# Kernel optimization log

Hardware: AMD Instinct MI355X
Metric: run time of the kernel (lower is better)

The kernel has to match this reference:

```python
import jax, jax.numpy as jnp
import numpy as np

MAX_SEQ_LEN = 2048
H, K = 16, 8
D_IN, D_OUT = 1024, 1024
D_H, D_O = D_IN // H, D_OUT // H


def _get_phi(L, K):
    # Hankel matrix Z[i,j] = 2 / ((i+j)^3 - (i+j) + 1e-7), 1-indexed
    e = np.arange(1, L + 1, dtype=np.float64)
    s = e[:, None] + e[None, :]
    Z = 2.0 / (s ** 3 - s + 1e-7)
    sigma, phi = np.linalg.eigh(Z)
    sigma, phi = sigma[-K:], phi[:, -K:]
    phi = phi * sigma ** 0.25
    return jnp.asarray(phi, dtype=jnp.float32)  # (L, K)


def setup_inputs() -> dict:
    key = jax.random.key(0)
    k_x, k_w, k_d = jax.random.split(key, 3)
    B, T = 4, 2048
    x = jax.random.normal(k_x, (B, T, D_IN), dtype=jnp.float32)
    # kaiming_uniform(a=sqrt(5)) on (H,K,d_h,d_o): fan_in = K*d_h*d_o, bound = 1/sqrt(fan_in)
    fan_in = K * D_H * D_O
    bound = 1.0 / np.sqrt(fan_in)
    weight = jax.random.uniform(k_w, (H, K, D_H, D_O), minval=-bound, maxval=bound, dtype=jnp.float32)
    # torch init is zeros; use small random so the score path is exercised
    diag = 0.02 * jax.random.normal(k_d, (K, D_IN), dtype=jnp.float32)
    phi = _get_phi(MAX_SEQ_LEN, K)
    return {"x": x, "weight": weight, "diag": diag, "phi": phi}


def reference(x, weight, diag, phi):
    B, T, _ = x.shape
    Hh, Kk, d_h, d_o = weight.shape
    # scores: (B, T, K) = phi[:T] broadcast + x @ diag^T
    scores = phi[:T][None, :, :] + jnp.einsum('bti,ki->btk', x, diag)
    xh = x.reshape(B, T, Hh, d_h).transpose(0, 2, 1, 3)  # (B, H, T, d_h)
    # per-head, per-expert GEMM -> (B, H, K, T, d_o)
    y = jnp.einsum('bhti,hkio->bhkto', xh, weight)
    # score-weighted combine over experts -> (B, T, H, d_o)
    y = jnp.einsum('bhkto,btk->btho', y, scores)
    return y.reshape(B, T, Hh * d_o)
```

## Files before the change

kernel.cpp:

```cpp
#include <hip/hip_runtime.h>
#include <hip/hip_bf16.h>

#define BT    8192
#define SEQ_T 2048
#define DIN   1024
#define NH    16
#define NK    8
#define DH    64
#define DO    64

typedef __bf16 bf16;
typedef __attribute__((ext_vector_type(8))) __bf16 bf16x8;
typedef __attribute__((ext_vector_type(4))) __bf16 bf16x4;
typedef __attribute__((ext_vector_type(4))) float floatx4;

__global__ __launch_bounds__(256) void prep_kernel(
    const float* __restrict__ x, const float* __restrict__ weight,
    const float* __restrict__ diag, const float* __restrict__ phi,
    float* __restrict__ scores_t, bf16* __restrict__ wt, bf16* __restrict__ xh)
{
  int blk = blockIdx.x, tid = threadIdx.x;
  if (blk < BT / 4) {
    int wave = tid >> 6, lane = tid & 63;
    int token = blk * 4 + wave;
    const floatx4* xr = (const floatx4*)(x + (size_t)token * DIN);
    const floatx4* dg = (const floatx4*)diag;
    floatx4 acc[NK];
#pragma unroll
    for (int k = 0; k < NK; k++) acc[k] = (floatx4){0.f, 0.f, 0.f, 0.f};
#pragma unroll
    for (int it = 0; it < 4; it++) {
      floatx4 xv = xr[it * 64 + lane];
      int col = it * 256 + lane * 4;
      int h = col >> 6, c = col & 63;
      bf16x4 cv;
      cv[0] = (bf16)xv[0]; cv[1] = (bf16)xv[1];
      cv[2] = (bf16)xv[2]; cv[3] = (bf16)xv[3];
      *(bf16x4*)(xh + ((size_t)h * BT + token) * 64 + c) = cv;
#pragma unroll
      for (int k = 0; k < NK; k++) {
        floatx4 dv = dg[k * 256 + it * 64 + lane];
        acc[k] += xv * dv;
      }
    }
    float r[NK];
#pragma unroll
    for (int k = 0; k < NK; k++)
      r[k] = (acc[k][0] + acc[k][1]) + (acc[k][2] + acc[k][3]);
#pragma unroll
    for (int k = 0; k < NK; k++) {
      float v = r[k];
#pragma unroll
      for (int off = 32; off >= 1; off >>= 1) v += __shfl_xor(v, off, 64);
      r[k] = v;
    }
    if (lane == 0) {
      int t = token & (SEQ_T - 1);
#pragma unroll
      for (int k = 0; k < NK; k++)
        scores_t[(size_t)k * BT + token] = phi[t * NK + k] + r[k];
    }
  } else {
    __shared__ bf16 tile[64 * 68];
    int hk = blk - BT / 4;
    const float* wsrc = weight + (size_t)hk * DH * DO;
#pragma unroll
    for (int it = 0; it < 4; it++) {
      int idx = it * 1024 + tid * 4;
      int i = idx >> 6, o = idx & 63;
      floatx4 v = *(const floatx4*)(wsrc + idx);
#pragma unroll
      for (int r = 0; r < 4; r++)
        tile[(o + r) * 68 + i] = (bf16)v[r];
    }
    __syncthreads();
#pragma unroll
    for (int it = 0; it < 4; it++) {
      int idx = it * 1024 + tid * 4;
      int o2 = idx >> 6, i2 = idx & 63;
      bf16x4 v = *(const bf16x4*)&tile[o2 * 68 + i2];
      *(bf16x4*)(wt + (size_t)hk * 4096 + idx) = v;
    }
  }
}

__global__ __launch_bounds__(256, 3) void moe_kernel(
    const bf16* __restrict__ xh, const bf16* __restrict__ wt,
    const float* __restrict__ scores_t, float* __restrict__ out)
{
  __shared__ bf16  xl[128 * 64];
  __shared__ bf16  wl[256 * 64];
  __shared__ float sl[NK * 128];

  int bid = blockIdx.x;
  int g  = bid >> 5;
  int h  = (bid >> 1) & 15;
  int nh = bid & 1;
  int tid = threadIdx.x, lane = tid & 63, w = tid >> 6;
  int l15 = lane & 15, q = lane >> 4;

  {
    const bf16* xs = xh + ((size_t)h * BT + g * 128) * 64;
#pragma unroll
    for (int it = 0; it < 4; it++) {
      int idx = it * 256 + tid;
      int row = idx >> 3, c = idx & 7, pc = c ^ (row & 7);
      bf16x8 v = *(const bf16x8*)(xs + idx * 8);
      *(bf16x8*)(xl + row * 64 + pc * 8) = v;
    }
  }
  {
#pragma unroll
    for (int it = 0; it < 8; it++) {
      int idx = it * 256 + tid;
      int R = idx >> 3, c = idx & 7;
      int e = R >> 5, o = R & 31;
      bf16x8 v = *(const bf16x8*)(wt + ((size_t)(h * NK + e) * DO + nh * 32 + o) * 64 + c * 8);
      int pc = c ^ (R & 7);
      *(bf16x8*)(wl + R * 64 + pc * 8) = v;
    }
  }
  {
    int k = tid >> 5, t4 = (tid & 31) * 4;
    floatx4 v = *(const floatx4*)(scores_t + (size_t)k * BT + g * 128 + t4);
    *(floatx4*)(sl + k * 128 + t4) = v;
  }
  __syncthreads();

  int mh = w >> 1;
  int ns = w & 1;

  bf16x8 b[NK][2];
#pragma unroll
  for (int e = 0; e < NK; e++) {
    int R = e * 32 + ns * 16 + l15;
#pragma unroll
    for (int ki = 0; ki < 2; ki++) {
      int pc = (ki * 4 + q) ^ (R & 7);
      b[e][ki] = *(const bf16x8*)(wl + R * 64 + pc * 8);
    }
  }

#pragma unroll
  for (int m = 0; m < 4; m++) {
    int tr = mh * 64 + m * 16;
    int row = tr + l15;
    int p0 = q ^ (row & 7), p1 = (q + 4) ^ (row & 7);
    bf16x8 a0 = *(const bf16x8*)(xl + row * 64 + p0 * 8);
    bf16x8 a1 = *(const bf16x8*)(xl + row * 64 + p1 * 8);
    floatx4 y = (floatx4){0.f, 0.f, 0.f, 0.f};
#pragma unroll
    for (int e = 0; e < NK; e++) {
      floatx4 s4 = *(const floatx4*)(sl + e * 128 + tr + q * 4);
      floatx4 z = (floatx4){0.f, 0.f, 0.f, 0.f};
      z = __builtin_amdgcn_mfma_f32_16x16x32_bf16(a0, b[e][0], z, 0, 0, 0);
      z = __builtin_amdgcn_mfma_f32_16x16x32_bf16(a1, b[e][1], z, 0, 0, 0);
      y += s4 * z;
    }
    int orow = g * 128 + tr + q * 4;
    float* op = out + (size_t)orow * (NH * DO) + h * DO + nh * 32 + ns * 16 + l15;
#pragma unroll
    for (int r = 0; r < 4; r++)
      op[(size_t)r * (NH * DO)] = y[r];
  }
}

extern "C" void kernel_launch(void* const* d_in, const int* in_sizes, int n_in,
                              void* d_out, int out_size, void* d_ws, size_t ws_size,
                              hipStream_t stream) {
  const float* x      = (const float*)d_in[0];
  const float* weight = (const float*)d_in[1];
  const float* diag   = (const float*)d_in[2];
  const float* phi    = (const float*)d_in[3];
  float* out = (float*)d_out;

  bf16*  wt       = (bf16*)d_ws;
  float* scores_t = (float*)((char*)d_ws + (2u << 20));
  bf16*  xh       = (bf16*)((char*)d_ws + (4u << 20));

  prep_kernel<<<BT / 4 + NH * NK, 256, 0, stream>>>(x, weight, diag, phi,
                                                    scores_t, wt, xh);
  moe_kernel<<<64 * NH * 2, 256, 0, stream>>>(xh, wt, scores_t, out);
}
```

Baseline: 108.6 us.

## Make MoE blocks persistent over four token tiles with double-buffered prefetch

Each moe_kernel block now handles four 128-token chunks instead of one, so the expert weight tile is loaded into shared memory once and reused across them. The next chunk's x and scores are prefetched into registers and written to a second LDS buffer while the current chunk computes. Block IDs are also remapped so that neighbouring blocks land on different XCDs, and launch bounds drop to 2 blocks per CU. Grid size falls from 2048 to 512 blocks, which reduces weight reloads and exposed load latency but risks lower occupancy and less parallelism.

```diff
diff --git a/kernel.cpp b/kernel.cpp
--- a/kernel.cpp
+++ b/kernel.cpp
@@ -84,52 +84,55 @@
   }
 }
 
-__global__ __launch_bounds__(256, 3) void moe_kernel(
+__global__ __launch_bounds__(256, 2) void moe_kernel(
     const bf16* __restrict__ xh, const bf16* __restrict__ wt,
     const float* __restrict__ scores_t, float* __restrict__ out)
 {
-  __shared__ bf16  xl[128 * 64];
   __shared__ bf16  wl[256 * 64];
-  __shared__ float sl[NK * 128];
-
-  int bid = blockIdx.x;
-  int g  = bid >> 5;
-  int h  = (bid >> 1) & 15;
-  int nh = bid & 1;
+  __shared__ bf16  xl[2][128 * 64];
+  __shared__ float sl[2][NK * 128];
+
+  int lid = ((blockIdx.x & 7) << 6) | (blockIdx.x >> 3);
+  int nh    = lid & 1;
+  int chunk = (lid >> 1) & 15;
+  int h     = lid >> 5;
   int tid = threadIdx.x, lane = tid & 63, w = tid >> 6;
   int l15 = lane & 15, q = lane >> 4;
 
-  {
-    const bf16* xs = xh + ((size_t)h * BT + g * 128) * 64;
-#pragma unroll
-    for (int it = 0; it < 4; it++) {
-      int idx = it * 256 + tid;
-      int row = idx >> 3, c = idx & 7, pc = c ^ (row & 7);
-      bf16x8 v = *(const bf16x8*)(xs + idx * 8);
-      *(bf16x8*)(xl + row * 64 + pc * 8) = v;
-    }
-  }
-  {
-#pragma unroll
-    for (int it = 0; it < 8; it++) {
-      int idx = it * 256 + tid;
-      int R = idx >> 3, c = idx & 7;
-      int e = R >> 5, o = R & 31;
-      bf16x8 v = *(const bf16x8*)(wt + ((size_t)(h * NK + e) * DO + nh * 32 + o) * 64 + c * 8);
-      int pc = c ^ (R & 7);
-      *(bf16x8*)(wl + R * 64 + pc * 8) = v;
-    }
-  }
-  {
-    int k = tid >> 5, t4 = (tid & 31) * 4;
-    floatx4 v = *(const floatx4*)(scores_t + (size_t)k * BT + g * 128 + t4);
-    *(floatx4*)(sl + k * 128 + t4) = v;
-  }
+  const bf16*  xs = xh + ((size_t)h * BT + chunk * 512) * 64;
+  const float* ss = scores_t + chunk * 512;
+  int sk = tid >> 5, st4 = (tid & 31) * 4;
+
+  bf16x8 wv[8];
+#pragma unroll
+  for (int it = 0; it < 8; it++) {
+    int idx = it * 256 + tid, R = idx >> 3, c = idx & 7;
+    int e = R >> 5, o = R & 31;
+    wv[it] = *(const bf16x8*)(wt +
+        (((size_t)(h * NK + e)) * DO + nh * 32 + o) * 64 + c * 8);
+  }
+  bf16x8 xv[4];
+#pragma unroll
+  for (int it = 0; it < 4; it++)
+    xv[it] = *(const bf16x8*)(xs + (it * 256 + tid) * 8);
+  floatx4 sv = *(const floatx4*)(ss + (size_t)sk * BT + st4);
+
+#pragma unroll
+  for (int it = 0; it < 8; it++) {
+    int idx = it * 256 + tid, R = idx >> 3, c = idx & 7;
+    int pc = c ^ (R & 7);
+    *(bf16x8*)(wl + R * 64 + pc * 8) = wv[it];
+  }
+#pragma unroll
+  for (int it = 0; it < 4; it++) {
+    int idx = it * 256 + tid, row = idx >> 3, c = idx & 7, pc = c ^ (row & 7);
+    *(bf16x8*)(xl[0] + row * 64 + pc * 8) = xv[it];
+  }
+  *(floatx4*)(sl[0] + sk * 128 + st4) = sv;
   __syncthreads();
 
   int mh = w >> 1;
   int ns = w & 1;
-
   bf16x8 b[NK][2];
 #pragma unroll
   for (int e = 0; e < NK; e++) {
@@ -142,26 +145,59 @@
   }
 
 #pragma unroll
-  for (int m = 0; m < 4; m++) {
-    int tr = mh * 64 + m * 16;
-    int row = tr + l15;
-    int p0 = q ^ (row & 7), p1 = (q + 4) ^ (row & 7);
-    bf16x8 a0 = *(const bf16x8*)(xl + row * 64 + p0 * 8);
-    bf16x8 a1 = *(const bf16x8*)(xl + row * 64 + p1 * 8);
-    floatx4 y = (floatx4){0.f, 0.f, 0.f, 0.f};
-#pragma unroll
-    for (int e = 0; e < NK; e++) {
-      floatx4 s4 = *(const floatx4*)(sl + e * 128 + tr + q * 4);
-      floatx4 z = (floatx4){0.f, 0.f, 0.f, 0.f};
-      z = __builtin_amdgcn_mfma_f32_16x16x32_bf16(a0, b[e][0], z, 0, 0, 0);
-      z = __builtin_amdgcn_mfma_f32_16x16x32_bf16(a1, b[e][1], z, 0, 0, 0);
-      y += s4 * z;
-    }
-    int orow = g * 128 + tr + q * 4;
-    float* op = out + (size_t)orow * (NH * DO) + h * DO + nh * 32 + ns * 16 + l15;
-#pragma unroll
-    for (int r = 0; r < 4; r++)
-      op[(size_t)r * (NH * DO)] = y[r];
+  for (int i = 0; i < 4; i++) {
+    const bf16*  xlc = xl[i & 1];
+    const float* slc = sl[i & 1];
+
+    if (i < 3) {
+#pragma unroll
+      for (int it = 0; it < 4; it++)
+        xv[it] = *(const bf16x8*)(xs + (i + 1) * (128 * 64) +
+                                  (it * 256 + tid) * 8);
+      sv = *(const floatx4*)(ss + (size_t)sk * BT + (i + 1) * 128 + st4);
+    }
+
+    floatx4 yy[4];
+#pragma unroll
+    for (int m = 0; m < 4; m++) {
+      int tr = mh * 64 + m * 16;
+      int row = tr + l15;
+      int p0 = q ^ (row & 7), p1 = (q + 4) ^ (row & 7);
+      bf16x8 a0 = *(const bf16x8*)(xlc + row * 64 + p0 * 8);
+      bf16x8 a1 = *(const bf16x8*)(xlc + row * 64 + p1 * 8);
+      floatx4 y = (floatx4){0.f, 0.f, 0.f, 0.f};
+#pragma unroll
+      for (int e = 0; e < NK; e++) {
+        floatx4 s4 = *(const floatx4*)(slc + e * 128 + tr + q * 4);
+        floatx4 z = (floatx4){0.f, 0.f, 0.f, 0.f};
+        z = __builtin_amdgcn_mfma_f32_16x16x32_bf16(a0, b[e][0], z, 0, 0, 0);
+        z = __builtin_amdgcn_mfma_f32_16x16x32_bf16(a1, b[e][1], z, 0, 0, 0);
+        y += s4 * z;
+      }
+      yy[m] = y;
+    }
+
+    if (i < 3) {
+#pragma unroll
+      for (int it = 0; it < 4; it++) {
+        int idx = it * 256 + tid, row = idx >> 3, c = idx & 7;
+        int pc = c ^ (row & 7);
+        *(bf16x8*)(xl[(i + 1) & 1] + row * 64 + pc * 8) = xv[it];
+      }
+      *(floatx4*)(sl[(i + 1) & 1] + sk * 128 + st4) = sv;
+      __syncthreads();
+    }
+
+#pragma unroll
+    for (int m = 0; m < 4; m++) {
+      int tr = mh * 64 + m * 16;
+      int orow = (chunk * 4 + i) * 128 + tr + q * 4;
+      float* op = out + (size_t)orow * (NH * DO) + h * DO +
+                  nh * 32 + ns * 16 + l15;
+#pragma unroll
+      for (int r = 0; r < 4; r++)
+        op[(size_t)r * (NH * DO)] = yy[m][r];
+    }
   }
 }
 
@@ -180,5 +216,5 @@
 
   prep_kernel<<<BT / 4 + NH * NK, 256, 0, stream>>>(x, weight, diag, phi,
                                                     scores_t, wt, xh);
-  moe_kernel<<<64 * NH * 2, 256, 0, stream>>>(xh, wt, scores_t, out);
+  moe_kernel<<<512, 256, 0, stream>>>(xh, wt, scores_t, out);
 }
```

Measured after the change: 110.0 us. No clear change (+1.3%).

## Pre-swizzle LDS images in prep and load via direct global-to-LDS DMA

Applied to the files above, without the earlier changes.

The prep kernel now writes x and weight already in the XOR-swizzled per-block LDS layout, so the MoE kernel can copy them with contiguous global_load_lds 16-byte transfers that skip the register round-trip. Scores are loaded the same way. The block index is also permuted so that consecutive blocks land on different XCDs, which changes L2 locality. This removes VGPR staging and address arithmetic from the load phase, but it relies on how global_load_lds places data for each lane. It also assumes the 16-byte LDS load is supported on this target.

```diff
diff --git a/kernel.cpp b/kernel.cpp
--- a/kernel.cpp
+++ b/kernel.cpp
@@ -14,15 +14,22 @@
 typedef __attribute__((ext_vector_type(4))) __bf16 bf16x4;
 typedef __attribute__((ext_vector_type(4))) float floatx4;
 
+#define GLOAD_LDS16(gp, lp)                                        \
+  __builtin_amdgcn_global_load_lds(                                \
+      (__attribute__((address_space(1))) const void*)(gp),         \
+      (__attribute__((address_space(3))) void*)(lp), 16, 0, 0)
+
 __global__ __launch_bounds__(256) void prep_kernel(
     const float* __restrict__ x, const float* __restrict__ weight,
     const float* __restrict__ diag, const float* __restrict__ phi,
-    float* __restrict__ scores_t, bf16* __restrict__ wt, bf16* __restrict__ xh)
+    float* __restrict__ scores_t, bf16* __restrict__ wimg,
+    bf16* __restrict__ ximg)
 {
   int blk = blockIdx.x, tid = threadIdx.x;
   if (blk < BT / 4) {
     int wave = tid >> 6, lane = tid & 63;
     int token = blk * 4 + wave;
+    int row = token & 127, gg = token >> 7;
     const floatx4* xr = (const floatx4*)(x + (size_t)token * DIN);
     const floatx4* dg = (const floatx4*)diag;
     floatx4 acc[NK];
@@ -36,7 +43,8 @@
       bf16x4 cv;
       cv[0] = (bf16)xv[0]; cv[1] = (bf16)xv[1];
       cv[2] = (bf16)xv[2]; cv[3] = (bf16)xv[3];
-      *(bf16x4*)(xh + ((size_t)h * BT + token) * 64 + c) = cv;
+      int a = (((c >> 3) ^ (row & 7)) << 3) + (c & 7);
+      *(bf16x4*)(ximg + ((size_t)(gg * 16 + h) * 128 + row) * 64 + a) = cv;
 #pragma unroll
       for (int k = 0; k < NK; k++) {
         floatx4 dv = dg[k * 256 + it * 64 + lane];
@@ -63,6 +71,7 @@
   } else {
     __shared__ bf16 tile[64 * 68];
     int hk = blk - BT / 4;
+    int h = hk >> 3, k = hk & 7;
     const float* wsrc = weight + (size_t)hk * DH * DO;
 #pragma unroll
     for (int it = 0; it < 4; it++) {
@@ -79,13 +88,15 @@
       int idx = it * 1024 + tid * 4;
       int o2 = idx >> 6, i2 = idx & 63;
       bf16x4 v = *(const bf16x4*)&tile[o2 * 68 + i2];
-      *(bf16x4*)(wt + (size_t)hk * 4096 + idx) = v;
+      int nh = o2 >> 5, o = o2 & 31, R = k * 32 + o;
+      int a = (((i2 >> 3) ^ (R & 7)) << 3) + (i2 & 7);
+      *(bf16x4*)(wimg + ((size_t)(h * 2 + nh) * 256 + R) * 64 + a) = v;
     }
   }
 }
 
 __global__ __launch_bounds__(256, 3) void moe_kernel(
-    const bf16* __restrict__ xh, const bf16* __restrict__ wt,
+    const bf16* __restrict__ ximg, const bf16* __restrict__ wimg,
     const float* __restrict__ scores_t, float* __restrict__ out)
 {
   __shared__ bf16  xl[128 * 64];
@@ -93,37 +104,28 @@
   __shared__ float sl[NK * 128];
 
   int bid = blockIdx.x;
-  int g  = bid >> 5;
-  int h  = (bid >> 1) & 15;
-  int nh = bid & 1;
+  int lid = ((bid & 7) << 8) | (bid >> 3);
+  int g  = lid >> 5;
+  int h  = (lid >> 1) & 15;
+  int nh = lid & 1;
   int tid = threadIdx.x, lane = tid & 63, w = tid >> 6;
   int l15 = lane & 15, q = lane >> 4;
 
   {
-    const bf16* xs = xh + ((size_t)h * BT + g * 128) * 64;
+    const bf16* xs = ximg + (size_t)(g * 16 + h) * 8192;
 #pragma unroll
-    for (int it = 0; it < 4; it++) {
-      int idx = it * 256 + tid;
-      int row = idx >> 3, c = idx & 7, pc = c ^ (row & 7);
-      bf16x8 v = *(const bf16x8*)(xs + idx * 8);
-      *(bf16x8*)(xl + row * 64 + pc * 8) = v;
-    }
+    for (int it = 0; it < 4; it++)
+      GLOAD_LDS16(xs + it * 2048 + tid * 8, xl + it * 2048 + tid * 8);
   }
   {
+    const bf16* ws = wimg + (size_t)(h * 2 + nh) * 16384;
 #pragma unroll
-    for (int it = 0; it < 8; it++) {
-      int idx = it * 256 + tid;
-      int R = idx >> 3, c = idx & 7;
-      int e = R >> 5, o = R & 31;
-      bf16x8 v = *(const bf16x8*)(wt + ((size_t)(h * NK + e) * DO + nh * 32 + o) * 64 + c * 8);
-      int pc = c ^ (R & 7);
-      *(bf16x8*)(wl + R * 64 + pc * 8) = v;
-    }
+    for (int it = 0; it < 8; it++)
+      GLOAD_LDS16(ws + it * 2048 + tid * 8, wl + it * 2048 + tid * 8);
   }
   {
-    int k = tid >> 5, t4 = (tid & 31) * 4;
-    floatx4 v = *(const floatx4*)(scores_t + (size_t)k * BT + g * 128 + t4);
-    *(floatx4*)(sl + k * 128 + t4) = v;
+    const float* ss = scores_t + (size_t)(tid >> 5) * BT + g * 128 + (tid & 31) * 4;
+    GLOAD_LDS16(ss, sl + tid * 4);
   }
   __syncthreads();
 
@@ -174,11 +176,11 @@
   const float* phi    = (const float*)d_in[3];
   float* out = (float*)d_out;
 
-  bf16*  wt       = (bf16*)d_ws;
+  bf16*  wimg     = (bf16*)d_ws;
   float* scores_t = (float*)((char*)d_ws + (2u << 20));
-  bf16*  xh       = (bf16*)((char*)d_ws + (4u << 20));
+  bf16*  ximg     = (bf16*)((char*)d_ws + (4u << 20));
 
   prep_kernel<<<BT / 4 + NH * NK, 256, 0, stream>>>(x, weight, diag, phi,
-                                                    scores_t, wt, xh);
-  moe_kernel<<<64 * NH * 2, 256, 0, stream>>>(xh, wt, scores_t, out);
+                                                    scores_t, wimg, ximg);
+  moe_kernel<<<64 * NH * 2, 256, 0, stream>>>(ximg, wimg, scores_t, out);
 }
```

Result: no change. 108.6 us (+0.0%).
